# Kernel tuning notes

Measured on AMD Instinct MI355X. Metric: run time of the kernel, lower is better.

## Reference

```python
import jax, jax.numpy as jnp
import numpy as np

ALPHA = 5.0

def setup_inputs() -> dict:
    key = jax.random.key(0)
    k1, k2 = jax.random.split(key)
    pred_points = jax.random.normal(k1, (4, 8192, 2), dtype=jnp.float32)
    gt_points = jax.random.normal(k2, (4, 8192, 2), dtype=jnp.float32)
    return {"pred_points": pred_points, "gt_points": gt_points}

def reference(pred_points, gt_points):
    # pairwise euclidean distances: (N, M, K)
    diff = pred_points[:, :, None, :] - gt_points[:, None, :, :]
    d = jnp.sqrt(jnp.sum(diff * diff, axis=-1))
    # soft-min via logsumexp along each axis (matches torch: no 1/alpha scaling)
    softmin_s_t = -jax.nn.logsumexp(-ALPHA * d, axis=1)  # (N, K)
    softmin_t_s = -jax.nn.logsumexp(-ALPHA * d, axis=2)  # (N, M)
    return softmin_s_t.mean() + softmin_t_s.mean()
```

## Files before the change

### kernel.cpp

```cpp
#include <hip/hip_runtime.h>

#define N_B    4
#define M_PTS  8192
#define K_PTS  8192
#define CCHUNK 1024
#define NTILE  (CCHUNK / 32)

#define FS    (7.21347520444481703f * 8388608.0f)
#define EXPA  1064879260.0f
#define SQB   0x1FBD1DF5u
#define LN2   0.69314718055994531f

typedef _Float16 f16x8 __attribute__((ext_vector_type(8)));
typedef float    f32x16 __attribute__((ext_vector_type(16)));

__device__ __forceinline__ f16x8 mk_b(uint2 v) {
    union { uint4 u; f16x8 h; } w;
    w.u = make_uint4(v.x, v.y, 0u, 0u);
    return w.h;
}

__global__ __launch_bounds__(256, 6) void softhaus_pair(
    const float* __restrict__ pred, const float* __restrict__ gt,
    float* __restrict__ row_sum, float* __restrict__ col_sum)
{
    __shared__ uint2 bfr[CCHUNK + 32];
    __shared__ float col_acc[CCHUNK];

    const int n    = blockIdx.z;
    const int rb   = blockIdx.x;
    const int cc   = blockIdx.y;
    const int tid  = threadIdx.x;
    const int lane = tid & 63;
    const int wv   = tid >> 6;
    const int l31  = lane & 31;

    const float2* P = (const float2*)pred + (size_t)n * M_PTS;
    const float2* G = (const float2*)gt   + (size_t)n * K_PTS;
    const int cbase = cc * CCHUNK;

    for (int i = tid; i < CCHUNK; i += 256) {
        const float2 g = G[cbase + i];
        const float ng = fmaf(g.x, g.x, g.y * g.y);
        union { _Float16 h[4]; uint2 u; } w;
        w.h[0] = (_Float16)g.x; w.h[1] = (_Float16)g.y;
        w.h[2] = (_Float16)1.0f; w.h[3] = (_Float16)ng;
        bfr[i] = w.u;
    }
    for (int i = tid; i < CCHUNK; i += 256) col_acc[i] = 0.0f;
    if (tid < 32) bfr[CCHUNK + tid] = make_uint2(0u, 0u);

    const int wrow0 = rb * 128 + wv * 32;
    const float2 p = P[wrow0 + l31];
    f16x8 a = {};
    if (lane < 32) {
        a[0] = (_Float16)(-2.0f * p.x);
        a[1] = (_Float16)(-2.0f * p.y);
        a[2] = (_Float16)fmaf(p.x, p.x, p.y * p.y);
        a[3] = (_Float16)1.0f;
    }

    __syncthreads();

    float rs[16];
    #pragma unroll
    for (int r = 0; r < 16; ++r) rs[r] = 0.0f;

    const unsigned bstride = (lane < 32) ? 32u : 0u;
    const unsigned bbase   = (lane < 32) ? (unsigned)l31
                                         : (unsigned)(CCHUNK + l31);
    const int toff = wv * (NTILE / 4);
    const f32x16 zacc = {};

    for (int t = 0; t < NTILE; ++t) {
        const int tp = (t + toff) & (NTILE - 1);
        const uint2 bv = bfr[bbase + (unsigned)tp * bstride];
        const f32x16 acc =
            __builtin_amdgcn_mfma_f32_32x32x16_f16(a, mk_b(bv), zacc, 0, 0, 0);

        float c = 0.0f;
        #pragma unroll
        for (int q = 0; q < 4; ++q) {
            float e0, e1, e2, e3;
            {
                const float s = fmaxf(acc[4*q+0], 0.0f);
                e0 = __uint_as_float((unsigned)(int)fmaf(
                    __uint_as_float((__float_as_uint(s) >> 1) + SQB), -FS, EXPA));
                const float s1 = fmaxf(acc[4*q+1], 0.0f);
                e1 = __uint_as_float((unsigned)(int)fmaf(
                    __uint_as_float((__float_as_uint(s1) >> 1) + SQB), -FS, EXPA));
                const float s2 = fmaxf(acc[4*q+2], 0.0f);
                e2 = __uint_as_float((unsigned)(int)fmaf(
                    __uint_as_float((__float_as_uint(s2) >> 1) + SQB), -FS, EXPA));
                const float s3 = fmaxf(acc[4*q+3], 0.0f);
                e3 = __uint_as_float((unsigned)(int)fmaf(
                    __uint_as_float((__float_as_uint(s3) >> 1) + SQB), -FS, EXPA));
            }
            rs[4*q+0] += e0; rs[4*q+1] += e1;
            rs[4*q+2] += e2; rs[4*q+3] += e3;
            c += (e0 + e1) + (e2 + e3);
        }
        c += __shfl_xor(c, 32);
        if (lane < 32)
            atomicAdd(&col_acc[tp * 32 + l31], c);
    }

    #pragma unroll
    for (int r = 0; r < 16; ++r) {
        #pragma unroll
        for (int m = 1; m <= 16; m <<= 1)
            rs[r] += __shfl_xor(rs[r], m, 32);
    }
    if (l31 == 0) {
        const int half4 = (lane >> 5) << 2;
        float* rsum = row_sum + (size_t)n * M_PTS;
        #pragma unroll
        for (int r = 0; r < 16; ++r) {
            const int row = wrow0 + (r & 3) + ((r >> 2) << 3) + half4;
            atomicAdd(&rsum[row], rs[r]);
        }
    }

    __syncthreads();
    for (int i = tid; i < CCHUNK; i += 256)
        atomicAdd(&col_sum[(size_t)n * K_PTS + cbase + i], col_acc[i]);
}

__global__ __launch_bounds__(256) void softhaus_finalize(
    const float* __restrict__ sums, float* __restrict__ out)
{
    const int total  = N_B * M_PTS + N_B * K_PTS;
    const int idx    = blockIdx.x * blockDim.x + threadIdx.x;
    const int stride = gridDim.x * blockDim.x;

    float acc = 0.0f;
    for (int i = idx; i < total; i += stride)
        acc -= __builtin_amdgcn_logf(sums[i]) * LN2;

    #pragma unroll
    for (int off = 32; off > 0; off >>= 1)
        acc += __shfl_down(acc, off);

    __shared__ float wsum[4];
    const int lane = threadIdx.x & 63;
    const int wv   = threadIdx.x >> 6;
    if (lane == 0) wsum[wv] = acc;
    __syncthreads();
    if (threadIdx.x == 0) {
        float b = wsum[0] + wsum[1] + wsum[2] + wsum[3];
        atomicAdd(out, b * (1.0f / (N_B * M_PTS)));
    }
}

extern "C" void kernel_launch(void* const* d_in, const int* in_sizes, int n_in,
                              void* d_out, int out_size, void* d_ws, size_t ws_size,
                              hipStream_t stream) {
    const float* pred = (const float*)d_in[0];
    const float* gt   = (const float*)d_in[1];
    float* ws = (float*)d_ws;

    const size_t acc_bytes = (size_t)(N_B * M_PTS + N_B * K_PTS) * sizeof(float);
    hipMemsetAsync(d_ws, 0, acc_bytes, stream);
    hipMemsetAsync(d_out, 0, sizeof(float), stream);

    dim3 grid(M_PTS / 128, K_PTS / CCHUNK, N_B);
    softhaus_pair<<<grid, 256, 0, stream>>>(pred, gt, ws, ws + (size_t)N_B * M_PTS);
    softhaus_finalize<<<64, 256, 0, stream>>>(ws, (float*)d_out);
}
```

Before: 75.43 us.

## Software-pipeline MFMA tiles and split column accumulators per half-wave

Issues the MFMA for the next tile before post-processing the previous one, so matrix and vector work can overlap. Replaces the cross-half shuffle and masked atomic with per-half-wave column accumulators in LDS that are summed at the end. Packs row accumulation into float2 vectors. This costs more LDS and register pressure from two live accumulators.

```diff
diff --git a/kernel.cpp b/kernel.cpp
--- a/kernel.cpp
+++ b/kernel.cpp
@@ -11,8 +11,9 @@
 #define SQB   0x1FBD1DF5u
 #define LN2   0.69314718055994531f
 
-typedef _Float16 f16x8 __attribute__((ext_vector_type(8)));
+typedef _Float16 f16x8  __attribute__((ext_vector_type(8)));
 typedef float    f32x16 __attribute__((ext_vector_type(16)));
+typedef float    v2f    __attribute__((ext_vector_type(2)));
 
 __device__ __forceinline__ f16x8 mk_b(uint2 v) {
     union { uint4 u; f16x8 h; } w;
@@ -20,12 +21,33 @@
     return w.h;
 }
 
+__device__ __forceinline__ void post_tile(const f32x16& acc, int tp,
+                                          v2f* rs2, float* col_half, int l31)
+{
+    v2f e2[8];
+    #pragma unroll
+    for (int q = 0; q < 8; ++q) {
+        const float s0 = fmaxf(acc[2*q+0], 0.0f);
+        const float s1 = fmaxf(acc[2*q+1], 0.0f);
+        v2f e;
+        e.x = __uint_as_float((unsigned)(int)fmaf(
+                 __uint_as_float((__float_as_uint(s0) >> 1) + SQB), -FS, EXPA));
+        e.y = __uint_as_float((unsigned)(int)fmaf(
+                 __uint_as_float((__float_as_uint(s1) >> 1) + SQB), -FS, EXPA));
+        e2[q] = e;
+        rs2[q] += e;
+    }
+    const v2f t = ((e2[0]+e2[1]) + (e2[2]+e2[3]))
+                + ((e2[4]+e2[5]) + (e2[6]+e2[7]));
+    atomicAdd(&col_half[tp * 32 + l31], t.x + t.y);
+}
+
 __global__ __launch_bounds__(256, 6) void softhaus_pair(
     const float* __restrict__ pred, const float* __restrict__ gt,
     float* __restrict__ row_sum, float* __restrict__ col_sum)
 {
-    __shared__ uint2 bfr[CCHUNK + 32];
-    __shared__ float col_acc[CCHUNK];
+    __shared__ uint2 bfr[CCHUNK];
+    __shared__ float col_acc[2 * CCHUNK];
 
     const int n    = blockIdx.z;
     const int rb   = blockIdx.x;
@@ -47,8 +69,9 @@
         w.h[2] = (_Float16)1.0f; w.h[3] = (_Float16)ng;
         bfr[i] = w.u;
     }
-    for (int i = tid; i < CCHUNK; i += 256) col_acc[i] = 0.0f;
-    if (tid < 32) bfr[CCHUNK + tid] = make_uint2(0u, 0u);
+    #pragma unroll
+    for (int i = 0; i < 2 * CCHUNK / 256; ++i)
+        col_acc[tid + i * 256] = 0.0f;
 
     const int wrow0 = rb * 128 + wv * 32;
     const float2 p = P[wrow0 + l31];
@@ -62,49 +85,42 @@
 
     __syncthreads();
 
+    v2f rs2[8];
+    #pragma unroll
+    for (int q = 0; q < 8; ++q) { rs2[q].x = 0.0f; rs2[q].y = 0.0f; }
+
+    float* col_half = col_acc + ((lane >= 32) ? CCHUNK : 0);
+    const int toff = wv * 8;
+    const f32x16 zacc = {};
+
+    int tpA = toff;
+    f32x16 accA = __builtin_amdgcn_mfma_f32_32x32x16_f16(
+        a, mk_b(bfr[tpA * 32 + l31]), zacc, 0, 0, 0);
+
+    #pragma unroll 2
+    for (int t = 0; t < NTILE - 2; t += 2) {
+        const int tpB = (t + 1 + toff) & (NTILE - 1);
+        f32x16 accB = __builtin_amdgcn_mfma_f32_32x32x16_f16(
+            a, mk_b(bfr[tpB * 32 + l31]), zacc, 0, 0, 0);
+        post_tile(accA, tpA, rs2, col_half, l31);
+
+        const int tpN = (t + 2 + toff) & (NTILE - 1);
+        accA = __builtin_amdgcn_mfma_f32_32x32x16_f16(
+            a, mk_b(bfr[tpN * 32 + l31]), zacc, 0, 0, 0);
+        post_tile(accB, tpB, rs2, col_half, l31);
+        tpA = tpN;
+    }
+    {
+        const int tpB = (NTILE - 1 + toff) & (NTILE - 1);
+        f32x16 accB = __builtin_amdgcn_mfma_f32_32x32x16_f16(
+            a, mk_b(bfr[tpB * 32 + l31]), zacc, 0, 0, 0);
+        post_tile(accA, tpA, rs2, col_half, l31);
+        post_tile(accB, tpB, rs2, col_half, l31);
+    }
+
     float rs[16];
     #pragma unroll
-    for (int r = 0; r < 16; ++r) rs[r] = 0.0f;
-
-    const unsigned bstride = (lane < 32) ? 32u : 0u;
-    const unsigned bbase   = (lane < 32) ? (unsigned)l31
-                                         : (unsigned)(CCHUNK + l31);
-    const int toff = wv * (NTILE / 4);
-    const f32x16 zacc = {};
-
-    for (int t = 0; t < NTILE; ++t) {
-        const int tp = (t + toff) & (NTILE - 1);
-        const uint2 bv = bfr[bbase + (unsigned)tp * bstride];
-        const f32x16 acc =
-            __builtin_amdgcn_mfma_f32_32x32x16_f16(a, mk_b(bv), zacc, 0, 0, 0);
-
-        float c = 0.0f;
-        #pragma unroll
-        for (int q = 0; q < 4; ++q) {
-            float e0, e1, e2, e3;
-            {
-                const float s = fmaxf(acc[4*q+0], 0.0f);
-                e0 = __uint_as_float((unsigned)(int)fmaf(
-                    __uint_as_float((__float_as_uint(s) >> 1) + SQB), -FS, EXPA));
-                const float s1 = fmaxf(acc[4*q+1], 0.0f);
-                e1 = __uint_as_float((unsigned)(int)fmaf(
-                    __uint_as_float((__float_as_uint(s1) >> 1) + SQB), -FS, EXPA));
-                const float s2 = fmaxf(acc[4*q+2], 0.0f);
-                e2 = __uint_as_float((unsigned)(int)fmaf(
-                    __uint_as_float((__float_as_uint(s2) >> 1) + SQB), -FS, EXPA));
-                const float s3 = fmaxf(acc[4*q+3], 0.0f);
-                e3 = __uint_as_float((unsigned)(int)fmaf(
-                    __uint_as_float((__float_as_uint(s3) >> 1) + SQB), -FS, EXPA));
-            }
-            rs[4*q+0] += e0; rs[4*q+1] += e1;
-            rs[4*q+2] += e2; rs[4*q+3] += e3;
-            c += (e0 + e1) + (e2 + e3);
-        }
-        c += __shfl_xor(c, 32);
-        if (lane < 32)
-            atomicAdd(&col_acc[tp * 32 + l31], c);
-    }
-
+    for (int q = 0; q < 8; ++q) { rs[2*q] = rs2[q].x; rs[2*q+1] = rs2[q].y; }
     #pragma unroll
     for (int r = 0; r < 16; ++r) {
         #pragma unroll
@@ -123,7 +139,8 @@
 
     __syncthreads();
     for (int i = tid; i < CCHUNK; i += 256)
-        atomicAdd(&col_sum[(size_t)n * K_PTS + cbase + i], col_acc[i]);
+        atomicAdd(&col_sum[(size_t)n * K_PTS + cbase + i],
+                  col_acc[i] + col_acc[CCHUNK + i]);
 }
 
 __global__ __launch_bounds__(256) void softhaus_finalize(
```

After: 108.8 us. 1.44x slower.
